# Kernel optimization log

Measured on AMD Instinct MI355X. Metric: run time of the kernel, lower is better.

The kernel has to match this reference:

```python
import jax, jax.numpy as jnp
import numpy as np

NUM_HEADS = 32
NUM_KV_HEADS = 8
HEAD_DIM = 128
WINDOW = 512
NUM_META = 4


def _swa_sink_mask(S):
    # allowed = causal & (within sliding window OR sink/meta token)
    i = jnp.arange(S)[:, None]   # q_idx
    j = jnp.arange(S)[None, :]   # kv_idx
    return (i >= j) & (((i - j) <= WINDOW) | (j < NUM_META))


def setup_inputs() -> dict:
    key = jax.random.key(0)
    k1, k2, k3 = jax.random.split(key, 3)
    B, S = 1, 2048
    return {
        "query_states": jax.random.normal(k1, (B, S, NUM_HEADS * HEAD_DIM), dtype=jnp.float32),
        "key_states": jax.random.normal(k2, (B, S, NUM_KV_HEADS * HEAD_DIM), dtype=jnp.float32),
        "value_states": jax.random.normal(k3, (B, S, NUM_KV_HEADS * HEAD_DIM), dtype=jnp.float32),
    }


def reference(query_states, key_states, value_states):
    B, S, _ = query_states.shape
    n_rep = NUM_HEADS // NUM_KV_HEADS
    # [B, H, S, D]
    q = query_states.reshape(B, S, NUM_HEADS, HEAD_DIM).transpose(0, 2, 1, 3)
    k = key_states.reshape(B, S, NUM_KV_HEADS, HEAD_DIM).transpose(0, 2, 1, 3)
    v = value_states.reshape(B, S, NUM_KV_HEADS, HEAD_DIM).transpose(0, 2, 1, 3)
    # repeat_kv: interleaved repeat along head dim (GQA)
    k = jnp.repeat(k, n_rep, axis=1)
    v = jnp.repeat(v, n_rep, axis=1)

    scale = 1.0 / jnp.sqrt(jnp.float32(HEAD_DIM))  # flex_attention default scale
    scores = jnp.einsum("bhqd,bhkd->bhqk", q, k) * scale
    mask = _swa_sink_mask(S)  # [S, S], every row has q_idx==kv_idx allowed
    scores = jnp.where(mask[None, None], scores, -jnp.inf)
    attn = jax.nn.softmax(scores, axis=-1)
    out = jnp.einsum("bhqk,bhkd->bhqd", attn, v)
    return out.transpose(0, 2, 1, 3).reshape(B, S, NUM_HEADS * HEAD_DIM)
```

## Files before the change

kernel.cpp:

```cpp
#include <hip/hip_runtime.h>
#include <math.h>

typedef __attribute__((ext_vector_type(8))) short bf16x8;
typedef __attribute__((ext_vector_type(16))) float f32x16;

#define WIN 512
#define META 4
#define KSTR 136
#define VSTR 72
#define QSCALE (0.08838834764831845f * 1.4426950408889634f)
#define MFIX2 20.197730572445487f

union U8 { int4 i4; bf16x8 bf; };

static __device__ __forceinline__ unsigned bf16_rne(float x) {
  unsigned u = __float_as_uint(x);
  return (u + 0x7FFFu + ((u >> 16) & 1u)) >> 16;
}
static __device__ __forceinline__ unsigned pk2_rne(float a, float b) {
  return bf16_rne(a) | (bf16_rne(b) << 16);
}
static __device__ __forceinline__ unsigned pk2_tr(float a, float b) {
  return (__float_as_uint(a) >> 16) | (__float_as_uint(b) & 0xFFFF0000u);
}

__global__ __launch_bounds__(256, 2) void swa_fused(
    const float* __restrict__ Qg, const float* __restrict__ Kg,
    const float* __restrict__ Vg, float* __restrict__ Og)
{
  __shared__ __align__(16) unsigned short Ks[2][64 * KSTR];
  __shared__ __align__(16) unsigned short Vts[2][128 * VSTR];

  const int tid = threadIdx.x;
  const int lane = tid & 63, wid = tid >> 6;
  const int cl = lane & 31, hl = lane >> 5;
  const int bid = blockIdx.x;
  const int hk = bid & 7;
  const int bq = bid >> 3;
  const int qtile = (bq & 1) ? (63 - (bq >> 1)) : (bq >> 1);
  const int q0 = qtile * 32;
  const int h = hk * 4 + wid;

  const int sh = tid >> 5;
  const int sc = (tid & 31) * 4;
  const int dg = tid & 15;
  const int kq = tid >> 4;
  const int vchunk = 2 * (kq >> 2) + (kq & 1);
  const int vhalf  = (kq >> 1) & 1;

  int4 qf[8];
  {
    const float* qrow = Qg + (size_t)(q0 + cl) * 4096 + h * 128 + hl * 8;
    #pragma unroll
    for (int kc = 0; kc < 8; ++kc) {
      float4 x = *(const float4*)(qrow + kc * 16);
      float4 y = *(const float4*)(qrow + kc * 16 + 4);
      qf[kc] = make_int4(pk2_rne(x.x*QSCALE, x.y*QSCALE), pk2_rne(x.z*QSCALE, x.w*QSCALE),
                         pk2_rne(y.x*QSCALE, y.y*QSCALE), pk2_rne(y.z*QSCALE, y.w*QSCALE));
    }
  }

  f32x16 acc[4];
  #pragma unroll
  for (int nt = 0; nt < 4; ++nt)
    #pragma unroll
    for (int i = 0; i < 16; ++i) acc[nt][i] = 0.f;
  float lpA = 0.f, lpB = 0.f;

  const int jstart = (q0 > WIN) ? ((q0 - WIN) & ~63) : 0;
  const int sink = (jstart > 0) ? 1 : 0;
  const int niter = ((q0 + 31 - jstart) >> 6) + 1 + sink;

  float4 kreg[8], vreg[8];
  {
    const int jt0 = sink ? 0 : jstart;
    const float* kb = Kg + (size_t)jt0 * 1024 + hk * 128 + sc;
    #pragma unroll
    for (int it = 0; it < 8; ++it)
      kreg[it] = *(const float4*)(kb + (size_t)(it * 8 + sh) * 1024);
    const float* vb = Vg + (size_t)jt0 * 1024 + hk * 128 + dg * 8;
    #pragma unroll
    for (int i = 0; i < 4; ++i) {
      vreg[2*i]   = *(const float4*)(vb + (size_t)(4 * kq + i) * 1024);
      vreg[2*i+1] = *(const float4*)(vb + (size_t)(4 * kq + i) * 1024 + 4);
    }
  }

  for (int t = 0; t < niter; ++t) {
    const bool isSink = (sink != 0) && (t == 0);
    const int jt = isSink ? 0 : jstart + ((t - sink) << 6);
    const bool needMask = (jt + 63 > q0) || (q0 + 31 - jt > WIN);
    const int cb = t & 1;
    unsigned short* Kb = Ks[cb];
    unsigned short* Vb = Vts[cb];

    #pragma unroll
    for (int it = 0; it < 8; ++it) {
      float4 v = kreg[it];
      *(uint2*)(Kb + (it * 8 + sh) * KSTR + sc) =
          make_uint2(pk2_tr(v.x, v.y), pk2_tr(v.z, v.w));
    }
    #pragma unroll
    for (int e = 0; e < 8; ++e) {
      const int d = dg * 8 + e;
      const int half = e >> 2, c = e & 3;
      const float* f0 = (const float*)&vreg[0 + half];
      const float* f1 = (const float*)&vreg[2 + half];
      const float* f2 = (const float*)&vreg[4 + half];
      const float* f3 = (const float*)&vreg[6 + half];
      *(uint2*)(Vb + d * VSTR + ((vchunk ^ (dg & 7)) << 3) + (vhalf << 2)) =
          make_uint2(pk2_tr(f0[c], f1[c]), pk2_tr(f2[c], f3[c]));
    }
    __syncthreads();

    if (t + 1 < niter) {
      const int jn = jstart + ((t + 1 - sink) << 6);
      const float* kb = Kg + (size_t)jn * 1024 + hk * 128 + sc;
      #pragma unroll
      for (int it = 0; it < 8; ++it)
        kreg[it] = *(const float4*)(kb + (size_t)(it * 8 + sh) * 1024);
      const float* vb = Vg + (size_t)jn * 1024 + hk * 128 + dg * 8;
      #pragma unroll
      for (int i = 0; i < 4; ++i) {
        vreg[2*i]   = *(const float4*)(vb + (size_t)(4 * kq + i) * 1024);
        vreg[2*i+1] = *(const float4*)(vb + (size_t)(4 * kq + i) * 1024 + 4);
      }
    }

    f32x16 s0v, s1v;
    #pragma unroll
    for (int i = 0; i < 16; ++i) { s0v[i] = 0.f; s1v[i] = 0.f; }
    __builtin_amdgcn_s_setprio(1);
    if (isSink) {
      #pragma unroll
      for (int kc = 0; kc < 8; ++kc) {
        U8 b; b.i4 = qf[kc];
        U8 a0; a0.i4 = *(const int4*)(Kb + cl * KSTR + kc * 16 + hl * 8);
        s0v = __builtin_amdgcn_mfma_f32_32x32x16_bf16(a0.bf, b.bf, s0v, 0, 0, 0);
      }
    } else {
      #pragma unroll
      for (int kc = 0; kc < 8; ++kc) {
        U8 b; b.i4 = qf[kc];
        U8 a0; a0.i4 = *(const int4*)(Kb + cl * KSTR + kc * 16 + hl * 8);
        s0v = __builtin_amdgcn_mfma_f32_32x32x16_bf16(a0.bf, b.bf, s0v, 0, 0, 0);
        U8 a1; a1.i4 = *(const int4*)(Kb + (32 + cl) * KSTR + kc * 16 + hl * 8);
        s1v = __builtin_amdgcn_mfma_f32_32x32x16_bf16(a1.bf, b.bf, s1v, 0, 0, 0);
      }
    }
    __builtin_amdgcn_s_setprio(0);

    unsigned pu0[16], pu1[16];
    const int q = q0 + cl;
    #pragma unroll
    for (int ri = 0; ri < 16; ++ri) {
      const int koff = (ri & 3) + 8 * (ri >> 2) + 4 * hl;
      bool ok0 = true, ok1 = true;
      if (needMask) {
        const int k0v = jt + koff, k1v = jt + 32 + koff;
        ok0 = (q >= k0v) && (((q - k0v) <= WIN) || (k0v < META));
        ok1 = (q >= k1v) && (((q - k1v) <= WIN) || (k1v < META));
      }
      unsigned u0 = ok0 ? (__float_as_uint(__builtin_amdgcn_exp2f(s0v[ri] - MFIX2)) & 0xFFFF0000u) : 0u;
      pu0[ri] = u0;
      lpA += __uint_as_float(u0);
      if (!isSink) {
        unsigned u1 = ok1 ? (__float_as_uint(__builtin_amdgcn_exp2f(s1v[ri] - MFIX2)) & 0xFFFF0000u) : 0u;
        pu1[ri] = u1;
        lpB += __uint_as_float(u1);
      }
    }

    #define MKA(P, o) make_int4((P[(o)] >> 16) | P[(o)+1], (P[(o)+2] >> 16) | P[(o)+3], \
                                (P[(o)+4] >> 16) | P[(o)+5], (P[(o)+6] >> 16) | P[(o)+7])
    const int kcmax = isSink ? 1 : 4;
    __builtin_amdgcn_s_setprio(1);
    for (int kc = 0; kc < kcmax; ++kc) {
      U8 a;
      a.i4 = (kc == 0) ? MKA(pu0, 0) : (kc == 1) ? MKA(pu0, 8)
           : (kc == 2) ? MKA(pu1, 0) : MKA(pu1, 8);
      #pragma unroll
      for (int nt = 0; nt < 4; ++nt) {
        const int dim = nt * 32 + cl;
        U8 b; b.i4 = *(const int4*)(Vb + dim * VSTR + (((2 * kc + hl) ^ ((dim >> 3) & 7)) << 3));
        acc[nt] = __builtin_amdgcn_mfma_f32_32x32x16_bf16(a.bf, b.bf, acc[nt], 0, 0, 0);
      }
    }
    __builtin_amdgcn_s_setprio(0);
    #undef MKA
  }

  const float lp = lpA + lpB;
  const float ltot = lp + __shfl_xor(lp, 32);
  const float inv = __fdividef(1.0f, ltot);
  #pragma unroll
  for (int ri = 0; ri < 16; ++ri) {
    const int rl = (ri & 3) + 8 * (ri >> 2) + 4 * hl;
    const float invq = __shfl(inv, rl, 64);
    #pragma unroll
    for (int nt = 0; nt < 4; ++nt) {
      Og[(size_t)(q0 + rl) * 4096 + h * 128 + nt * 32 + cl] = acc[nt][ri] * invq;
    }
  }
}

extern "C" void kernel_launch(void* const* d_in, const int* in_sizes, int n_in,
                              void* d_out, int out_size, void* d_ws, size_t ws_size,
                              hipStream_t stream) {
  const float* Q = (const float*)d_in[0];
  const float* K = (const float*)d_in[1];
  const float* V = (const float*)d_in[2];
  float* O = (float*)d_out;
  hipLaunchKernelGGL(swa_fused, dim3(512), dim3(256), 0, stream, Q, K, V, O);
}
```

Before: 124.7 us.

## Double query tile per block to share K/V staging across eight waves

Each block now covers 64 query rows using 8 waves (two 32-row groups per head) instead of 32 rows with 4 waves. The grid shrinks to 256 blocks of 512 threads. Each K/V tile loaded from global memory and converted to bf16 in LDS now serves twice as many queries, halving K/V traffic and conversion work per query. The alternating heavy/light qtile ordering is dropped, and the upper wave group in a block may iterate over tiles it fully masks, so load balance and occupancy could suffer.

```diff
diff --git a/kernel.cpp b/kernel.cpp
--- a/kernel.cpp
+++ b/kernel.cpp
@@ -24,7 +24,7 @@
   return (__float_as_uint(a) >> 16) | (__float_as_uint(b) & 0xFFFF0000u);
 }
 
-__global__ __launch_bounds__(256, 2) void swa_fused(
+__global__ __launch_bounds__(512, 2) void swa_fused(
     const float* __restrict__ Qg, const float* __restrict__ Kg,
     const float* __restrict__ Vg, float* __restrict__ Og)
 {
@@ -37,20 +37,21 @@
   const int bid = blockIdx.x;
   const int hk = bid & 7;
   const int bq = bid >> 3;
-  const int qtile = (bq & 1) ? (63 - (bq >> 1)) : (bq >> 1);
-  const int q0 = qtile * 32;
-  const int h = hk * 4 + wid;
-
-  const int sh = tid >> 5;
-  const int sc = (tid & 31) * 4;
-  const int dg = tid & 15;
-  const int kq = tid >> 4;
+  const int q0 = bq << 6;
+  const int h = hk * 4 + (wid & 3);
+  const int qw0 = q0 + ((wid >> 2) << 5);
+
+  const int ksh = tid >> 5;
+  const int ksc = (tid & 31) * 4;
+  const int dgv = tid & 31;
+  const int kq = tid >> 5;
   const int vchunk = 2 * (kq >> 2) + (kq & 1);
   const int vhalf  = (kq >> 1) & 1;
+  const int vxor   = (dgv >> 1) & 7;
 
   int4 qf[8];
   {
-    const float* qrow = Qg + (size_t)(q0 + cl) * 4096 + h * 128 + hl * 8;
+    const float* qrow = Qg + (size_t)(qw0 + cl) * 4096 + h * 128 + hl * 8;
     #pragma unroll
     for (int kc = 0; kc < 8; ++kc) {
       float4 x = *(const float4*)(qrow + kc * 16);
@@ -69,62 +70,57 @@
 
   const int jstart = (q0 > WIN) ? ((q0 - WIN) & ~63) : 0;
   const int sink = (jstart > 0) ? 1 : 0;
-  const int niter = ((q0 + 31 - jstart) >> 6) + 1 + sink;
-
-  float4 kreg[8], vreg[8];
+  const int niter = ((q0 + 63 - jstart) >> 6) + 1 + sink;
+
+  float4 kreg[4], vreg[4];
   {
     const int jt0 = sink ? 0 : jstart;
-    const float* kb = Kg + (size_t)jt0 * 1024 + hk * 128 + sc;
-    #pragma unroll
-    for (int it = 0; it < 8; ++it)
-      kreg[it] = *(const float4*)(kb + (size_t)(it * 8 + sh) * 1024);
-    const float* vb = Vg + (size_t)jt0 * 1024 + hk * 128 + dg * 8;
-    #pragma unroll
-    for (int i = 0; i < 4; ++i) {
-      vreg[2*i]   = *(const float4*)(vb + (size_t)(4 * kq + i) * 1024);
-      vreg[2*i+1] = *(const float4*)(vb + (size_t)(4 * kq + i) * 1024 + 4);
-    }
+    const float* kb = Kg + (size_t)jt0 * 1024 + hk * 128 + ksc;
+    #pragma unroll
+    for (int it = 0; it < 4; ++it)
+      kreg[it] = *(const float4*)(kb + (size_t)(it * 16 + ksh) * 1024);
+    const float* vb = Vg + (size_t)jt0 * 1024 + hk * 128 + dgv * 4;
+    #pragma unroll
+    for (int i = 0; i < 4; ++i)
+      vreg[i] = *(const float4*)(vb + (size_t)(4 * kq + i) * 1024);
   }
 
   for (int t = 0; t < niter; ++t) {
     const bool isSink = (sink != 0) && (t == 0);
     const int jt = isSink ? 0 : jstart + ((t - sink) << 6);
-    const bool needMask = (jt + 63 > q0) || (q0 + 31 - jt > WIN);
+    const bool needMask = (jt + 63 > qw0) || (qw0 + 31 - jt > WIN);
     const int cb = t & 1;
     unsigned short* Kb = Ks[cb];
     unsigned short* Vb = Vts[cb];
 
     #pragma unroll
-    for (int it = 0; it < 8; ++it) {
+    for (int it = 0; it < 4; ++it) {
       float4 v = kreg[it];
-      *(uint2*)(Kb + (it * 8 + sh) * KSTR + sc) =
+      *(uint2*)(Kb + (it * 16 + ksh) * KSTR + ksc) =
           make_uint2(pk2_tr(v.x, v.y), pk2_tr(v.z, v.w));
     }
     #pragma unroll
-    for (int e = 0; e < 8; ++e) {
-      const int d = dg * 8 + e;
-      const int half = e >> 2, c = e & 3;
-      const float* f0 = (const float*)&vreg[0 + half];
-      const float* f1 = (const float*)&vreg[2 + half];
-      const float* f2 = (const float*)&vreg[4 + half];
-      const float* f3 = (const float*)&vreg[6 + half];
-      *(uint2*)(Vb + d * VSTR + ((vchunk ^ (dg & 7)) << 3) + (vhalf << 2)) =
-          make_uint2(pk2_tr(f0[c], f1[c]), pk2_tr(f2[c], f3[c]));
+    for (int e = 0; e < 4; ++e) {
+      const int d = dgv * 4 + e;
+      const float* f0 = (const float*)&vreg[0];
+      const float* f1 = (const float*)&vreg[1];
+      const float* f2 = (const float*)&vreg[2];
+      const float* f3 = (const float*)&vreg[3];
+      *(uint2*)(Vb + d * VSTR + ((vchunk ^ vxor) << 3) + (vhalf << 2)) =
+          make_uint2(pk2_tr(f0[e], f1[e]), pk2_tr(f2[e], f3[e]));
     }
     __syncthreads();
 
     if (t + 1 < niter) {
       const int jn = jstart + ((t + 1 - sink) << 6);
-      const float* kb = Kg + (size_t)jn * 1024 + hk * 128 + sc;
-      #pragma unroll
-      for (int it = 0; it < 8; ++it)
-        kreg[it] = *(const float4*)(kb + (size_t)(it * 8 + sh) * 1024);
-      const float* vb = Vg + (size_t)jn * 1024 + hk * 128 + dg * 8;
-      #pragma unroll
-      for (int i = 0; i < 4; ++i) {
-        vreg[2*i]   = *(const float4*)(vb + (size_t)(4 * kq + i) * 1024);
-        vreg[2*i+1] = *(const float4*)(vb + (size_t)(4 * kq + i) * 1024 + 4);
-      }
+      const float* kb = Kg + (size_t)jn * 1024 + hk * 128 + ksc;
+      #pragma unroll
+      for (int it = 0; it < 4; ++it)
+        kreg[it] = *(const float4*)(kb + (size_t)(it * 16 + ksh) * 1024);
+      const float* vb = Vg + (size_t)jn * 1024 + hk * 128 + dgv * 4;
+      #pragma unroll
+      for (int i = 0; i < 4; ++i)
+        vreg[i] = *(const float4*)(vb + (size_t)(4 * kq + i) * 1024);
     }
 
     f32x16 s0v, s1v;
@@ -151,7 +147,7 @@
     __builtin_amdgcn_s_setprio(0);
 
     unsigned pu0[16], pu1[16];
-    const int q = q0 + cl;
+    const int q = qw0 + cl;
     #pragma unroll
     for (int ri = 0; ri < 16; ++ri) {
       const int koff = (ri & 3) + 8 * (ri >> 2) + 4 * hl;
@@ -199,7 +195,7 @@
     const float invq = __shfl(inv, rl, 64);
     #pragma unroll
     for (int nt = 0; nt < 4; ++nt) {
-      Og[(size_t)(q0 + rl) * 4096 + h * 128 + nt * 32 + cl] = acc[nt][ri] * invq;
+      Og[(size_t)(qw0 + rl) * 4096 + h * 128 + nt * 32 + cl] = acc[nt][ri] * invq;
     }
   }
 }
@@ -211,5 +207,5 @@
   const float* K = (const float*)d_in[1];
   const float* V = (const float*)d_in[2];
   float* O = (float*)d_out;
-  hipLaunchKernelGGL(swa_fused, dim3(512), dim3(256), 0, stream, Q, K, V, O);
-}
+  hipLaunchKernelGGL(swa_fused, dim3(256), dim3(512), 0, stream, Q, K, V, O);
+}
```

After: 122.2 us. About the same (-2.0%).
